# Kernel tuning notes

Hardware: AMD Instinct MI355X
Metric: run time of the kernel (lower is better)

## Reference

```python
import jax, jax.numpy as jnp
import numpy as np

N_NODES = 50000
N_EDGES = 800000
DIM = 128
N_LAYERS = 3
N_GRAPHS = 64
NEG_SLOPE = 0.2


def setup_inputs() -> dict:
    key = jax.random.key(0)
    ks = jax.random.split(key, 9)
    x = jax.random.normal(ks[0], (N_NODES, DIM), dtype=jnp.float32)
    edge_index = jax.random.randint(ks[1], (2, N_EDGES), 0, N_NODES, dtype=jnp.int32)
    batch = jnp.sort(jax.random.randint(ks[2], (N_NODES,), 0, N_GRAPHS, dtype=jnp.int32))
    Ws = jax.random.normal(ks[3], (N_LAYERS, DIM, DIM), dtype=jnp.float32) / np.sqrt(DIM)
    att_src = jax.random.normal(ks[4], (N_LAYERS, DIM), dtype=jnp.float32) * 0.1
    att_dst = jax.random.normal(ks[5], (N_LAYERS, DIM), dtype=jnp.float32) * 0.1
    biases = jnp.zeros((N_LAYERS, DIM), dtype=jnp.float32)
    Wf = jax.random.normal(ks[6], (DIM, 1), dtype=jnp.float32) / np.sqrt(DIM)
    bf = jnp.zeros((1,), dtype=jnp.float32)
    return {"x": x, "edge_index": edge_index, "batch": batch, "Ws": Ws,
            "att_src": att_src, "att_dst": att_dst, "biases": biases,
            "Wf": Wf, "bf": bf}


def _gat_layer(x, src, dst, W, a_src, a_dst, b, n_nodes):
    # PyG GATConv, heads=1: linear transform, per-edge attention, softmax over
    # edges incoming to each dst node, scatter-add aggregation, bias.
    h = x @ W                                        # [N, H]
    alpha = jax.nn.leaky_relu(
        (h * a_src).sum(-1)[src] + (h * a_dst).sum(-1)[dst], NEG_SLOPE)  # [E]
    m = jax.ops.segment_max(alpha, dst, num_segments=n_nodes)
    e = jnp.exp(alpha - m[dst])
    s = jax.ops.segment_sum(e, dst, num_segments=n_nodes)
    w = e / (s[dst] + 1e-16)                         # softmax per dst-neighborhood
    out = jax.ops.segment_sum(w[:, None] * h[src], dst, num_segments=n_nodes)
    return out + b


def reference(x, edge_index, batch, Ws, att_src, att_dst, biases, Wf, bf):
    n_nodes = x.shape[0]
    loop = jnp.arange(n_nodes, dtype=edge_index.dtype)   # add_self_loops=True
    src = jnp.concatenate([edge_index[0], loop])
    dst = jnp.concatenate([edge_index[1], loop])
    for l in range(N_LAYERS):
        x = _gat_layer(x, src, dst, Ws[l], att_src[l], att_dst[l], biases[l], n_nodes)
        x = jax.nn.relu(x)
    pooled = jax.ops.segment_sum(x, batch, num_segments=N_GRAPHS)  # global_add_pool
    y = (pooled @ Wf + bf).squeeze(-1)               # [N_GRAPHS]
    return y
```

## Files before the change

kernel.cpp:

```cpp
#include <hip/hip_runtime.h>
#include <hip/hip_bf16.h>

#define N_NODES 50000
#define DIM 128
#define N_GRAPHS 64
#define E_RAW 800000
#define E_TOT 850000
#define NSLOT 1000000
#define E_CAP 1200000
#define NEG_SLOPE 0.2f
#define PAD_SENT 0xFFFF0000u

typedef unsigned int uint;
typedef unsigned short ushort;
typedef float v2f __attribute__((ext_vector_type(2)));
typedef short bf16x8 __attribute__((ext_vector_type(8)));
typedef float f32x4 __attribute__((ext_vector_type(4)));

__device__ __forceinline__ int pi_pos(int p) {
    return (p >> 3) + 32 * ((p >> 1) & 3) + 16 * (p & 1);
}

__device__ __forceinline__ ushort f2bf(float f) {
    uint u = __float_as_uint(f);
    u += 0x7fffu + ((u >> 16) & 1u);
    return (ushort)(u >> 16);
}

__global__ void init_kernel(int* deg, int* fillc, float* pooled) {
    int i = blockIdx.x * blockDim.x + threadIdx.x;
    if (i < N_NODES) { deg[i] = 0; fillc[i] = 0; }
    if (i < N_GRAPHS * DIM) pooled[i] = 0.f;
}

__global__ void csr_init_kernel(uint* __restrict__ csr) {
    int i = blockIdx.x * blockDim.x + threadIdx.x;
    if (i < NSLOT / 4) ((uint4*)csr)[i] = make_uint4(PAD_SENT, PAD_SENT, PAD_SENT, PAD_SENT);
}

__global__ void x2bf_kernel(const float* __restrict__ x, ushort* __restrict__ xb) {
    int i = blockIdx.x * blockDim.x + threadIdx.x;
    if (i >= N_NODES * DIM / 4) return;
    float4 v = ((const float4*)x)[i];
    ushort4 o;
    o.x = f2bf(v.x); o.y = f2bf(v.y); o.z = f2bf(v.z); o.w = f2bf(v.w);
    ((ushort4*)xb)[i] = o;
}

__global__ void wprep_kernel(const float* __restrict__ Ws, ushort* __restrict__ Wfrag) {
    int t = blockIdx.x * blockDim.x + threadIdx.x;
    if (t >= 3 * 32 * 64) return;
    int l = t >> 11;
    int rem = t & 2047;
    int chunk = rem >> 6, lane = rem & 63;
    int ks = chunk >> 3, nt = chunk & 7;
    int cc = lane & 15, gg = lane >> 4;
    const float* W = Ws + (size_t)l * DIM * DIM;
    ushort o[8];
#pragma unroll
    for (int j = 0; j < 8; ++j) {
        int kp = ks * 32 + gg * 8 + j;
        int kl = (l == 0) ? kp : pi_pos(kp);
        o[j] = f2bf(W[kl * DIM + nt * 16 + cc]);
    }
#pragma unroll
    for (int j = 0; j < 8; ++j) Wfrag[(size_t)t * 8 + j] = o[j];
}

__global__ void count_kernel(const int* __restrict__ ei, int* __restrict__ deg) {
    int e = blockIdx.x * blockDim.x + threadIdx.x;
    if (e >= E_TOT) return;
    int dst = (e < E_RAW) ? ei[E_RAW + e] : (e - E_RAW);
    atomicAdd(&deg[dst], 1);
}

__global__ void scan1_kernel(const int* __restrict__ deg, int* __restrict__ excl,
                             int* __restrict__ blksum, int n) {
    __shared__ int lds[256];
    int t = threadIdx.x;
    int i = blockIdx.x * 256 + t;
    int v = (i < n) ? ((deg[i] + 3) & ~3) : 0;
    lds[t] = v;
    __syncthreads();
    int incl = v;
    for (int off = 1; off < 256; off <<= 1) {
        int y = (t >= off) ? lds[t - off] : 0;
        __syncthreads();
        incl += y;
        lds[t] = incl;
        __syncthreads();
    }
    if (i < n) excl[i] = incl - v;
    if (t == 255) blksum[blockIdx.x] = incl;
}

__global__ void scan2_kernel(int* __restrict__ blksum, int* __restrict__ row_ptr, int nblk) {
    __shared__ int lds[256];
    int t = threadIdx.x;
    int v = (t < nblk) ? blksum[t] : 0;
    lds[t] = v;
    __syncthreads();
    int incl = v;
    for (int off = 1; off < 256; off <<= 1) {
        int y = (t >= off) ? lds[t - off] : 0;
        __syncthreads();
        incl += y;
        lds[t] = incl;
        __syncthreads();
    }
    if (t < nblk) blksum[t] = incl - v;
    if (t == nblk - 1) row_ptr[N_NODES] = incl;
}

__global__ void scan3_kernel(int* __restrict__ row_ptr, const int* __restrict__ blksum, int n) {
    int i = blockIdx.x * blockDim.x + threadIdx.x;
    if (i < n) row_ptr[i] += blksum[i >> 8];
}

__global__ void fill_kernel(const int* __restrict__ ei, const int* __restrict__ row_ptr,
                            int* __restrict__ fillc, uint* __restrict__ csr) {
    int e = blockIdx.x * blockDim.x + threadIdx.x;
    if (e >= E_TOT) return;
    int src, dst;
    if (e < E_RAW) { src = ei[e]; dst = ei[E_RAW + e]; }
    else           { src = dst = e - E_RAW; }
    int slot = row_ptr[dst] + atomicAdd(&fillc[dst], 1);
    csr[slot] = (uint)src | ((uint)dst << 16);
}

__global__ __launch_bounds__(256) void gemm_mfma_kernel(
    const ushort* __restrict__ Xb, const ushort* __restrict__ Wfrag,
    const float* __restrict__ asrc, const float* __restrict__ adst,
    uint* __restrict__ Hb, float* __restrict__ s1, float* __restrict__ s2, int nrows) {
    int wv = threadIdx.x >> 6;
    int lane = threadIdx.x & 63;
    int c = lane & 15, g = lane >> 4;
    int row0 = blockIdx.x * 64 + wv * 16;

    int arow = row0 + c;
    if (arow >= nrows) arow = nrows - 1;
    const ushort* xrow = Xb + (size_t)arow * DIM;

    f32x4 acc[8];
#pragma unroll
    for (int nt = 0; nt < 8; ++nt) acc[nt] = (f32x4)(0.f);

#pragma unroll
    for (int ks = 0; ks < 4; ++ks) {
        bf16x8 afrag = *(const bf16x8*)(xrow + ks * 32 + g * 8);
#pragma unroll
        for (int nt = 0; nt < 8; ++nt) {
            bf16x8 bfrag = *(const bf16x8*)(Wfrag + ((size_t)(ks * 8 + nt) * 64 + lane) * 8);
            acc[nt] = __builtin_amdgcn_mfma_f32_16x16x32_bf16(afrag, bfrag, acc[nt], 0, 0, 0);
        }
    }

    float a1[8], a2[8];
#pragma unroll
    for (int nt = 0; nt < 8; ++nt) { a1[nt] = asrc[c + 16 * nt]; a2[nt] = adst[c + 16 * nt]; }

#pragma unroll
    for (int r = 0; r < 4; ++r) {
        int outrow = row0 + g * 4 + r;
        bool valid = outrow < nrows;
        if (valid) {
            int w0 = __builtin_amdgcn_cvt_pk_fp8_f32(acc[0][r], acc[1][r], 0, false);
            w0     = __builtin_amdgcn_cvt_pk_fp8_f32(acc[2][r], acc[3][r], w0, true);
            int w1 = __builtin_amdgcn_cvt_pk_fp8_f32(acc[4][r], acc[5][r], 0, false);
            w1     = __builtin_amdgcn_cvt_pk_fp8_f32(acc[6][r], acc[7][r], w1, true);
            *(uint2*)&Hb[(size_t)outrow * 32 + c * 2] = make_uint2((uint)w0, (uint)w1);
        }
        float p1 = 0.f, p2 = 0.f;
#pragma unroll
        for (int nt = 0; nt < 8; ++nt) {
            p1 = fmaf(acc[nt][r], a1[nt], p1);
            p2 = fmaf(acc[nt][r], a2[nt], p2);
        }
#pragma unroll
        for (int m = 1; m < 16; m <<= 1) { p1 += __shfl_xor(p1, m); p2 += __shfl_xor(p2, m); }
        if (c == 0 && valid) { s1[outrow] = p1; s2[outrow] = p2; }
    }
}

__global__ __launch_bounds__(256) void ew_kernel(
    const uint* __restrict__ csr, const float* __restrict__ s1,
    const float* __restrict__ s2, uint* __restrict__ cw) {
    int i = blockIdx.x * blockDim.x + threadIdx.x;
    if (i >= NSLOT / 4) return;
    uint4 e = ((const uint4*)csr)[i];
    uint ev[4] = {e.x, e.y, e.z, e.w};
    uint ov[4];
#pragma unroll
    for (int j = 0; j < 4; ++j) {
        uint dv = ev[j] >> 16;
        uint sv = ev[j] & 0xFFFFu;
        uint out = 0u;
        if (dv != 0xFFFFu) {
            float al = s1[sv] + s2[dv];
            al = fmaxf(al, NEG_SLOPE * al);
            float wv = __expf(al);
            out = sv | ((uint)f2bf(wv) << 16);
        }
        ov[j] = out;
    }
    ((uint4*)cw)[i] = make_uint4(ov[0], ov[1], ov[2], ov[3]);
}

__global__ __launch_bounds__(256) void agg_kernel(
    const uint2* __restrict__ Hb2, const uint* __restrict__ cw,
    const int* __restrict__ row_ptr, const float* __restrict__ bias,
    ushort* __restrict__ Xout, const int* __restrict__ batch,
    float* __restrict__ pooled, int pool_flag, int ngroups) {
    int gw = (blockIdx.x * blockDim.x + threadIdx.x) >> 6;
    int lane = threadIdx.x & 63;
    if (gw >= ngroups) return;
    int node0 = gw * 8;
    int ql = lane & 15;
    int grp = lane >> 4;

    int4 rpa = *(const int4*)&row_ptr[node0];
    int4 rpb = *(const int4*)&row_ptr[node0 + 4];
    int rp8 = row_ptr[node0 + 8];

    int p0 = 8 * ql + 2 * grp;
    float2 b2;
    b2.x = bias[pi_pos(p0)];
    b2.y = bias[pi_pos(p0) + 16];

    int ba0 = 0, ba1 = 0, ba2 = 0, ba3 = 0, ba4 = 0, ba5 = 0, ba6 = 0, ba7 = 0;
    if (pool_flag) {
        int4 bqa = *(const int4*)&batch[node0];
        int4 bqb = *(const int4*)&batch[node0 + 4];
        ba0 = bqa.x; ba1 = bqa.y; ba2 = bqa.z; ba3 = bqa.w;
        ba4 = bqb.x; ba5 = bqb.y; ba6 = bqb.z; ba7 = bqb.w;
    }

    auto seg = [&](int beg, int end, int bk, int node) {
        float a0 = 0.f, a1 = 0.f, a2 = 0.f, a3 = 0.f;
        float a4 = 0.f, a5 = 0.f, a6 = 0.f, a7 = 0.f, ws = 0.f;

        for (int s = beg; s < end; s += 16) {
            uint4 c0 = *(const uint4*)&cw[s];
            uint4 c1 = *(const uint4*)&cw[s + 4];
            uint4 c2 = *(const uint4*)&cw[s + 8];
            uint4 c3 = *(const uint4*)&cw[s + 12];

            uint e0 = (grp == 0) ? c0.x : (grp == 1) ? c0.y : (grp == 2) ? c0.z : c0.w;
            uint e1 = (grp == 0) ? c1.x : (grp == 1) ? c1.y : (grp == 2) ? c1.z : c1.w;
            uint e2 = (grp == 0) ? c2.x : (grp == 1) ? c2.y : (grp == 2) ? c2.z : c2.w;
            uint e3 = (grp == 0) ? c3.x : (grp == 1) ? c3.y : (grp == 2) ? c3.z : c3.w;
            e1 = (s + 4 + grp < end) ? e1 : 0u;
            e2 = (s + 8 + grp < end) ? e2 : 0u;
            e3 = (s + 12 + grp < end) ? e3 : 0u;

            uint2 h0 = Hb2[(e0 & 0xFFFFu) * 16u + (uint)ql];
            uint2 h1 = Hb2[(e1 & 0xFFFFu) * 16u + (uint)ql];
            uint2 h2 = Hb2[(e2 & 0xFFFFu) * 16u + (uint)ql];
            uint2 h3 = Hb2[(e3 & 0xFFFFu) * 16u + (uint)ql];

            float w0 = __uint_as_float(e0 & 0xFFFF0000u);
            float w1 = __uint_as_float(e1 & 0xFFFF0000u);
            float w2 = __uint_as_float(e2 & 0xFFFF0000u);
            float w3 = __uint_as_float(e3 & 0xFFFF0000u);

            v2f f;
            f = __builtin_amdgcn_cvt_pk_f32_fp8((int)h0.x, false); a0 = fmaf(w0, f.x, a0); a1 = fmaf(w0, f.y, a1);
            f = __builtin_amdgcn_cvt_pk_f32_fp8((int)h0.x, true);  a2 = fmaf(w0, f.x, a2); a3 = fmaf(w0, f.y, a3);
            f = __builtin_amdgcn_cvt_pk_f32_fp8((int)h0.y, false); a4 = fmaf(w0, f.x, a4); a5 = fmaf(w0, f.y, a5);
            f = __builtin_amdgcn_cvt_pk_f32_fp8((int)h0.y, true);  a6 = fmaf(w0, f.x, a6); a7 = fmaf(w0, f.y, a7);
            ws += w0;
            f = __builtin_amdgcn_cvt_pk_f32_fp8((int)h1.x, false); a0 = fmaf(w1, f.x, a0); a1 = fmaf(w1, f.y, a1);
            f = __builtin_amdgcn_cvt_pk_f32_fp8((int)h1.x, true);  a2 = fmaf(w1, f.x, a2); a3 = fmaf(w1, f.y, a3);
            f = __builtin_amdgcn_cvt_pk_f32_fp8((int)h1.y, false); a4 = fmaf(w1, f.x, a4); a5 = fmaf(w1, f.y, a5);
            f = __builtin_amdgcn_cvt_pk_f32_fp8((int)h1.y, true);  a6 = fmaf(w1, f.x, a6); a7 = fmaf(w1, f.y, a7);
            ws += w1;
            f = __builtin_amdgcn_cvt_pk_f32_fp8((int)h2.x, false); a0 = fmaf(w2, f.x, a0); a1 = fmaf(w2, f.y, a1);
            f = __builtin_amdgcn_cvt_pk_f32_fp8((int)h2.x, true);  a2 = fmaf(w2, f.x, a2); a3 = fmaf(w2, f.y, a3);
            f = __builtin_amdgcn_cvt_pk_f32_fp8((int)h2.y, false); a4 = fmaf(w2, f.x, a4); a5 = fmaf(w2, f.y, a5);
            f = __builtin_amdgcn_cvt_pk_f32_fp8((int)h2.y, true);  a6 = fmaf(w2, f.x, a6); a7 = fmaf(w2, f.y, a7);
            ws += w2;
            f = __builtin_amdgcn_cvt_pk_f32_fp8((int)h3.x, false); a0 = fmaf(w3, f.x, a0); a1 = fmaf(w3, f.y, a1);
            f = __builtin_amdgcn_cvt_pk_f32_fp8((int)h3.x, true);  a2 = fmaf(w3, f.x, a2); a3 = fmaf(w3, f.y, a3);
            f = __builtin_amdgcn_cvt_pk_f32_fp8((int)h3.y, false); a4 = fmaf(w3, f.x, a4); a5 = fmaf(w3, f.y, a5);
            f = __builtin_amdgcn_cvt_pk_f32_fp8((int)h3.y, true);  a6 = fmaf(w3, f.x, a6); a7 = fmaf(w3, f.y, a7);
            ws += w3;
        }

        a0 += __shfl_xor(a0, 16); a0 += __shfl_xor(a0, 32);
        a1 += __shfl_xor(a1, 16); a1 += __shfl_xor(a1, 32);
        a2 += __shfl_xor(a2, 16); a2 += __shfl_xor(a2, 32);
        a3 += __shfl_xor(a3, 16); a3 += __shfl_xor(a3, 32);
        a4 += __shfl_xor(a4, 16); a4 += __shfl_xor(a4, 32);
        a5 += __shfl_xor(a5, 16); a5 += __shfl_xor(a5, 32);
        a6 += __shfl_xor(a6, 16); a6 += __shfl_xor(a6, 32);
        a7 += __shfl_xor(a7, 16); a7 += __shfl_xor(a7, 32);
        ws += __shfl_xor(ws, 16); ws += __shfl_xor(ws, 32);

        float inv = 1.f / (ws + 1e-16f);
        float vx = (grp == 0) ? a0 : (grp == 1) ? a2 : (grp == 2) ? a4 : a6;
        float vy = (grp == 0) ? a1 : (grp == 1) ? a3 : (grp == 2) ? a5 : a7;
        vx = fmaxf(fmaf(vx, inv, b2.x), 0.f);
        vy = fmaxf(fmaf(vy, inv, b2.y), 0.f);

        if (pool_flag) {
            atomicAdd(&pooled[bk * DIM + p0], vx);
            atomicAdd(&pooled[bk * DIM + p0 + 1], vy);
        } else {
            ushort2 hb;
            hb.x = f2bf(vx);
            hb.y = f2bf(vy);
            ((ushort2*)Xout)[(size_t)node * 64 + (p0 >> 1)] = hb;
        }
    };

    seg(rpa.x, rpa.y, ba0, node0);
    seg(rpa.y, rpa.z, ba1, node0 + 1);
    seg(rpa.z, rpa.w, ba2, node0 + 2);
    seg(rpa.w, rpb.x, ba3, node0 + 3);
    seg(rpb.x, rpb.y, ba4, node0 + 4);
    seg(rpb.y, rpb.z, ba5, node0 + 5);
    seg(rpb.z, rpb.w, ba6, node0 + 6);
    seg(rpb.w, rp8,  ba7, node0 + 7);
}

__global__ void final_kernel(const float* __restrict__ pooled, const float* __restrict__ Wf,
                             const float* __restrict__ bf, float* __restrict__ y) {
    int wid = (blockIdx.x * blockDim.x + threadIdx.x) >> 6;
    int lane = threadIdx.x & 63;
    if (wid >= N_GRAPHS) return;
    float2 p = *(const float2*)&pooled[wid * DIM + 2 * lane];
    int cc = lane >> 2, ii = lane & 3;
    float wx = Wf[cc + 32 * ii];
    float wy = Wf[cc + 32 * ii + 16];
    float v = p.x * wx + p.y * wy;
    for (int off = 32; off; off >>= 1) v += __shfl_down(v, off);
    if (lane == 0) y[wid] = v + bf[0];
}

extern "C" void kernel_launch(void* const* d_in, const int* in_sizes, int n_in,
                              void* d_out, int out_size, void* d_ws, size_t ws_size,
                              hipStream_t stream) {
    const float* x       = (const float*)d_in[0];
    const int*   ei      = (const int*)d_in[1];
    const int*   batch   = (const int*)d_in[2];
    const float* Ws      = (const float*)d_in[3];
    const float* att_src = (const float*)d_in[4];
    const float* att_dst = (const float*)d_in[5];
    const float* biases  = (const float*)d_in[6];
    const float* Wf      = (const float*)d_in[7];
    const float* bf      = (const float*)d_in[8];
    float* y = (float*)d_out;

    char* p = (char*)d_ws;
    auto alloc = [&](size_t bytes) -> void* {
        void* r = (void*)p;
        p += (bytes + 255) & ~(size_t)255;
        return r;
    };
    ushort* xC     = (ushort*)alloc((size_t)(N_NODES + 64) * DIM * 2);
    ushort* xA     = (ushort*)alloc((size_t)(N_NODES + 64) * DIM * 2);
    uint*   Hb     = (uint*)alloc((size_t)N_NODES * 32 * 4);
    ushort* Wfrag  = (ushort*)alloc((size_t)3 * 32 * 64 * 8 * 2);
    uint*  csr     = (uint*)alloc((size_t)E_CAP * 4);
    uint*  cwbuf   = (uint*)alloc((size_t)E_CAP * 4);
    int*   deg     = (int*)alloc((size_t)N_NODES * 4);
    int*   fillc   = (int*)alloc((size_t)N_NODES * 4);
    int*   row_ptr = (int*)alloc((size_t)(N_NODES + 16) * 4);
    int*   blksum  = (int*)alloc(256 * 4);
    float* s1      = (float*)alloc((size_t)N_NODES * 4);
    float* s2      = (float*)alloc((size_t)(N_NODES + 8) * 4);
    float* pooled  = (float*)alloc((size_t)N_GRAPHS * DIM * 4);

    const int BN = 256;
    const int gN   = (N_NODES + BN - 1) / BN;
    const int gE   = (E_TOT + BN - 1) / BN;
    const int ngroups = N_NODES / 8;
    const int gAGG = (ngroups * 64 + BN - 1) / BN;
    const int nblk = gN;
    const int gCVT = (N_NODES * DIM / 4 + BN - 1) / BN;
    const int gGEMM = (N_NODES + 63) / 64;
    const int gEW  = (NSLOT / 4 + BN - 1) / BN;
    const int gCI  = (NSLOT / 4 + BN - 1) / BN;

    init_kernel<<<gN, BN, 0, stream>>>(deg, fillc, pooled);
    csr_init_kernel<<<gCI, BN, 0, stream>>>(csr);
    x2bf_kernel<<<gCVT, BN, 0, stream>>>(x, xC);
    wprep_kernel<<<(3 * 32 * 64 + BN - 1) / BN, BN, 0, stream>>>(Ws, Wfrag);
    count_kernel<<<gE, BN, 0, stream>>>(ei, deg);
    scan1_kernel<<<nblk, BN, 0, stream>>>(deg, row_ptr, blksum, N_NODES);
    scan2_kernel<<<1, BN, 0, stream>>>(blksum, row_ptr, nblk);
    scan3_kernel<<<gN, BN, 0, stream>>>(row_ptr, blksum, N_NODES);
    fill_kernel<<<gE, BN, 0, stream>>>(ei, row_ptr, fillc, csr);

    const ushort* xin = xC;
    ushort* xout = xA;
    for (int l = 0; l < 3; ++l) {
        const ushort* Wf_l = Wfrag + (size_t)l * 32 * 64 * 8;
        const float* as = att_src + (size_t)l * DIM;
        const float* ad = att_dst + (size_t)l * DIM;
        const float* b  = biases + (size_t)l * DIM;

        gemm_mfma_kernel<<<gGEMM, BN, 0, stream>>>(xin, Wf_l, as, ad, Hb, s1, s2, N_NODES);
        ew_kernel<<<gEW, BN, 0, stream>>>(csr, s1, s2, cwbuf);
        agg_kernel<<<gAGG, BN, 0, stream>>>((const uint2*)Hb, cwbuf, row_ptr, b,
                                            xout, batch, pooled,
                                            (l == 2) ? 1 : 0, ngroups);
        xin = xout;
        xout = (l == 0) ? xC : xA;
    }

    final_kernel<<<(N_GRAPHS * 64 + BN - 1) / BN, BN, 0, stream>>>(pooled, Wf, bf, y);
    (void)ws_size; (void)n_in; (void)in_sizes; (void)out_size;
}
```

Baseline: 350.1 us.

## Assign each 16-lane quarter-wave its own nodes in GAT aggregation

Each wave still covers 8 destination nodes, but now each 16-lane group handles two of them serially, reading 4 edges per iteration, instead of all 64 lanes cooperatively handling one node at a time. This drops the cross-group shuffle reductions and the lane-select logic, and each lane writes 8 contiguous bf16 outputs as one uint4 store. The cost is load imbalance between groups whose nodes have different degrees, and wasted padded slots if a segment's padding is shorter than 4 entries. The pooled atomics rise to 8 per lane per node.

```diff
diff --git a/kernel.cpp b/kernel.cpp
--- a/kernel.cpp
+++ b/kernel.cpp
@@ -209,7 +209,7 @@
 __global__ __launch_bounds__(256) void agg_kernel(
     const uint2* __restrict__ Hb2, const uint* __restrict__ cw,
     const int* __restrict__ row_ptr, const float* __restrict__ bias,
-    ushort* __restrict__ Xout, const int* __restrict__ batch,
+    uint4* __restrict__ Xout4, const int* __restrict__ batch,
     float* __restrict__ pooled, int pool_flag, int ngroups) {
     int gw = (blockIdx.x * blockDim.x + threadIdx.x) >> 6;
     int lane = threadIdx.x & 63;
@@ -222,105 +222,91 @@
     int4 rpb = *(const int4*)&row_ptr[node0 + 4];
     int rp8 = row_ptr[node0 + 8];
 
-    int p0 = 8 * ql + 2 * grp;
-    float2 b2;
-    b2.x = bias[pi_pos(p0)];
-    b2.y = bias[pi_pos(p0) + 16];
-
-    int ba0 = 0, ba1 = 0, ba2 = 0, ba3 = 0, ba4 = 0, ba5 = 0, ba6 = 0, ba7 = 0;
+    int begA = (grp == 0) ? rpa.x : (grp == 1) ? rpa.z : (grp == 2) ? rpb.x : rpb.z;
+    int midA = (grp == 0) ? rpa.y : (grp == 1) ? rpa.w : (grp == 2) ? rpb.y : rpb.w;
+    int endB = (grp == 0) ? rpa.z : (grp == 1) ? rpb.x : (grp == 2) ? rpb.z : rp8;
+    int nodeA = node0 + 2 * grp;
+
+    float b0 = bias[pi_pos(8 * ql + 0)], b1 = bias[pi_pos(8 * ql + 1)];
+    float b2 = bias[pi_pos(8 * ql + 2)], b3 = bias[pi_pos(8 * ql + 3)];
+    float b4 = bias[pi_pos(8 * ql + 4)], b5 = bias[pi_pos(8 * ql + 5)];
+    float b6 = bias[pi_pos(8 * ql + 6)], b7 = bias[pi_pos(8 * ql + 7)];
+
+    int bkA = 0, bkB = 0;
     if (pool_flag) {
         int4 bqa = *(const int4*)&batch[node0];
         int4 bqb = *(const int4*)&batch[node0 + 4];
-        ba0 = bqa.x; ba1 = bqa.y; ba2 = bqa.z; ba3 = bqa.w;
-        ba4 = bqb.x; ba5 = bqb.y; ba6 = bqb.z; ba7 = bqb.w;
+        bkA = (grp == 0) ? bqa.x : (grp == 1) ? bqa.z : (grp == 2) ? bqb.x : bqb.z;
+        bkB = (grp == 0) ? bqa.y : (grp == 1) ? bqa.w : (grp == 2) ? bqb.y : bqb.w;
     }
 
     auto seg = [&](int beg, int end, int bk, int node) {
         float a0 = 0.f, a1 = 0.f, a2 = 0.f, a3 = 0.f;
         float a4 = 0.f, a5 = 0.f, a6 = 0.f, a7 = 0.f, ws = 0.f;
 
-        for (int s = beg; s < end; s += 16) {
-            uint4 c0 = *(const uint4*)&cw[s];
-            uint4 c1 = *(const uint4*)&cw[s + 4];
-            uint4 c2 = *(const uint4*)&cw[s + 8];
-            uint4 c3 = *(const uint4*)&cw[s + 12];
-
-            uint e0 = (grp == 0) ? c0.x : (grp == 1) ? c0.y : (grp == 2) ? c0.z : c0.w;
-            uint e1 = (grp == 0) ? c1.x : (grp == 1) ? c1.y : (grp == 2) ? c1.z : c1.w;
-            uint e2 = (grp == 0) ? c2.x : (grp == 1) ? c2.y : (grp == 2) ? c2.z : c2.w;
-            uint e3 = (grp == 0) ? c3.x : (grp == 1) ? c3.y : (grp == 2) ? c3.z : c3.w;
-            e1 = (s + 4 + grp < end) ? e1 : 0u;
-            e2 = (s + 8 + grp < end) ? e2 : 0u;
-            e3 = (s + 12 + grp < end) ? e3 : 0u;
-
-            uint2 h0 = Hb2[(e0 & 0xFFFFu) * 16u + (uint)ql];
-            uint2 h1 = Hb2[(e1 & 0xFFFFu) * 16u + (uint)ql];
-            uint2 h2 = Hb2[(e2 & 0xFFFFu) * 16u + (uint)ql];
-            uint2 h3 = Hb2[(e3 & 0xFFFFu) * 16u + (uint)ql];
-
-            float w0 = __uint_as_float(e0 & 0xFFFF0000u);
-            float w1 = __uint_as_float(e1 & 0xFFFF0000u);
-            float w2 = __uint_as_float(e2 & 0xFFFF0000u);
-            float w3 = __uint_as_float(e3 & 0xFFFF0000u);
+        for (int s = beg; s < end; s += 4) {
+            uint4 c = *(const uint4*)&cw[s];
+
+            uint2 h0 = Hb2[(c.x & 0xFFFFu) * 16u + (uint)ql];
+            uint2 h1 = Hb2[(c.y & 0xFFFFu) * 16u + (uint)ql];
+            uint2 h2 = Hb2[(c.z & 0xFFFFu) * 16u + (uint)ql];
+            uint2 h3 = Hb2[(c.w & 0xFFFFu) * 16u + (uint)ql];
+            float w0 = __uint_as_float(c.x & 0xFFFF0000u);
+            float w1 = __uint_as_float(c.y & 0xFFFF0000u);
+            float w2 = __uint_as_float(c.z & 0xFFFF0000u);
+            float w3 = __uint_as_float(c.w & 0xFFFF0000u);
 
             v2f f;
             f = __builtin_amdgcn_cvt_pk_f32_fp8((int)h0.x, false); a0 = fmaf(w0, f.x, a0); a1 = fmaf(w0, f.y, a1);
             f = __builtin_amdgcn_cvt_pk_f32_fp8((int)h0.x, true);  a2 = fmaf(w0, f.x, a2); a3 = fmaf(w0, f.y, a3);
             f = __builtin_amdgcn_cvt_pk_f32_fp8((int)h0.y, false); a4 = fmaf(w0, f.x, a4); a5 = fmaf(w0, f.y, a5);
             f = __builtin_amdgcn_cvt_pk_f32_fp8((int)h0.y, true);  a6 = fmaf(w0, f.x, a6); a7 = fmaf(w0, f.y, a7);
-            ws += w0;
             f = __builtin_amdgcn_cvt_pk_f32_fp8((int)h1.x, false); a0 = fmaf(w1, f.x, a0); a1 = fmaf(w1, f.y, a1);
             f = __builtin_amdgcn_cvt_pk_f32_fp8((int)h1.x, true);  a2 = fmaf(w1, f.x, a2); a3 = fmaf(w1, f.y, a3);
             f = __builtin_amdgcn_cvt_pk_f32_fp8((int)h1.y, false); a4 = fmaf(w1, f.x, a4); a5 = fmaf(w1, f.y, a5);
             f = __builtin_amdgcn_cvt_pk_f32_fp8((int)h1.y, true);  a6 = fmaf(w1, f.x, a6); a7 = fmaf(w1, f.y, a7);
-            ws += w1;
             f = __builtin_amdgcn_cvt_pk_f32_fp8((int)h2.x, false); a0 = fmaf(w2, f.x, a0); a1 = fmaf(w2, f.y, a1);
             f = __builtin_amdgcn_cvt_pk_f32_fp8((int)h2.x, true);  a2 = fmaf(w2, f.x, a2); a3 = fmaf(w2, f.y, a3);
             f = __builtin_amdgcn_cvt_pk_f32_fp8((int)h2.y, false); a4 = fmaf(w2, f.x, a4); a5 = fmaf(w2, f.y, a5);
             f = __builtin_amdgcn_cvt_pk_f32_fp8((int)h2.y, true);  a6 = fmaf(w2, f.x, a6); a7 = fmaf(w2, f.y, a7);
-            ws += w2;
             f = __builtin_amdgcn_cvt_pk_f32_fp8((int)h3.x, false); a0 = fmaf(w3, f.x, a0); a1 = fmaf(w3, f.y, a1);
             f = __builtin_amdgcn_cvt_pk_f32_fp8((int)h3.x, true);  a2 = fmaf(w3, f.x, a2); a3 = fmaf(w3, f.y, a3);
             f = __builtin_amdgcn_cvt_pk_f32_fp8((int)h3.y, false); a4 = fmaf(w3, f.x, a4); a5 = fmaf(w3, f.y, a5);
             f = __builtin_amdgcn_cvt_pk_f32_fp8((int)h3.y, true);  a6 = fmaf(w3, f.x, a6); a7 = fmaf(w3, f.y, a7);
-            ws += w3;
-        }
-
-        a0 += __shfl_xor(a0, 16); a0 += __shfl_xor(a0, 32);
-        a1 += __shfl_xor(a1, 16); a1 += __shfl_xor(a1, 32);
-        a2 += __shfl_xor(a2, 16); a2 += __shfl_xor(a2, 32);
-        a3 += __shfl_xor(a3, 16); a3 += __shfl_xor(a3, 32);
-        a4 += __shfl_xor(a4, 16); a4 += __shfl_xor(a4, 32);
-        a5 += __shfl_xor(a5, 16); a5 += __shfl_xor(a5, 32);
-        a6 += __shfl_xor(a6, 16); a6 += __shfl_xor(a6, 32);
-        a7 += __shfl_xor(a7, 16); a7 += __shfl_xor(a7, 32);
-        ws += __shfl_xor(ws, 16); ws += __shfl_xor(ws, 32);
+            ws += (w0 + w1) + (w2 + w3);
+        }
 
         float inv = 1.f / (ws + 1e-16f);
-        float vx = (grp == 0) ? a0 : (grp == 1) ? a2 : (grp == 2) ? a4 : a6;
-        float vy = (grp == 0) ? a1 : (grp == 1) ? a3 : (grp == 2) ? a5 : a7;
-        vx = fmaxf(fmaf(vx, inv, b2.x), 0.f);
-        vy = fmaxf(fmaf(vy, inv, b2.y), 0.f);
+        float v0 = fmaxf(fmaf(a0, inv, b0), 0.f);
+        float v1 = fmaxf(fmaf(a1, inv, b1), 0.f);
+        float v2 = fmaxf(fmaf(a2, inv, b2), 0.f);
+        float v3 = fmaxf(fmaf(a3, inv, b3), 0.f);
+        float v4 = fmaxf(fmaf(a4, inv, b4), 0.f);
+        float v5 = fmaxf(fmaf(a5, inv, b5), 0.f);
+        float v6 = fmaxf(fmaf(a6, inv, b6), 0.f);
+        float v7 = fmaxf(fmaf(a7, inv, b7), 0.f);
 
         if (pool_flag) {
-            atomicAdd(&pooled[bk * DIM + p0], vx);
-            atomicAdd(&pooled[bk * DIM + p0 + 1], vy);
+            atomicAdd(&pooled[bk * DIM + 8 * ql + 0], v0);
+            atomicAdd(&pooled[bk * DIM + 8 * ql + 1], v1);
+            atomicAdd(&pooled[bk * DIM + 8 * ql + 2], v2);
+            atomicAdd(&pooled[bk * DIM + 8 * ql + 3], v3);
+            atomicAdd(&pooled[bk * DIM + 8 * ql + 4], v4);
+            atomicAdd(&pooled[bk * DIM + 8 * ql + 5], v5);
+            atomicAdd(&pooled[bk * DIM + 8 * ql + 6], v6);
+            atomicAdd(&pooled[bk * DIM + 8 * ql + 7], v7);
         } else {
-            ushort2 hb;
-            hb.x = f2bf(vx);
-            hb.y = f2bf(vy);
-            ((ushort2*)Xout)[(size_t)node * 64 + (p0 >> 1)] = hb;
+            uint4 o;
+            o.x = (uint)f2bf(v0) | ((uint)f2bf(v1) << 16);
+            o.y = (uint)f2bf(v2) | ((uint)f2bf(v3) << 16);
+            o.z = (uint)f2bf(v4) | ((uint)f2bf(v5) << 16);
+            o.w = (uint)f2bf(v6) | ((uint)f2bf(v7) << 16);
+            Xout4[(size_t)node * 16 + ql] = o;
         }
     };
 
-    seg(rpa.x, rpa.y, ba0, node0);
-    seg(rpa.y, rpa.z, ba1, node0 + 1);
-    seg(rpa.z, rpa.w, ba2, node0 + 2);
-    seg(rpa.w, rpb.x, ba3, node0 + 3);
-    seg(rpb.x, rpb.y, ba4, node0 + 4);
-    seg(rpb.y, rpb.z, ba5, node0 + 5);
-    seg(rpb.z, rpb.w, ba6, node0 + 6);
-    seg(rpb.w, rp8,  ba7, node0 + 7);
+    seg(begA, midA, bkA, nodeA);
+    seg(midA, endB, bkB, nodeA + 1);
 }
 
 __global__ void final_kernel(const float* __restrict__ pooled, const float* __restrict__ Wf,
@@ -403,7 +389,7 @@
         gemm_mfma_kernel<<<gGEMM, BN, 0, stream>>>(xin, Wf_l, as, ad, Hb, s1, s2, N_NODES);
         ew_kernel<<<gEW, BN, 0, stream>>>(csr, s1, s2, cwbuf);
         agg_kernel<<<gAGG, BN, 0, stream>>>((const uint2*)Hb, cwbuf, row_ptr, b,
-                                            xout, batch, pooled,
+                                            (uint4*)xout, batch, pooled,
                                             (l == 2) ? 1 : 0, ngroups);
         xin = xout;
         xout = (l == 0) ? xC : xA;
```

Result: slower. 589.2 us (+68.3%).
